# Kernel optimization log

Measured on AMD Instinct MI355X. Metric: run time of the kernel, lower is better.

The kernel has to match this reference:

```python
import jax, jax.numpy as jnp
import numpy as np

PAD_Y = 16
PAD_X = 16


def setup_inputs() -> dict:
    key = jax.random.key(0)
    k1, k2, k3, k4 = jax.random.split(key, 4)
    B, NLAM, H, W = 4, 96, 256, 256
    KS = 15
    cube = jax.random.normal(k1, (B, NLAM, H, W), dtype=jnp.float32)
    # per-(ksequence, wavelength) dispersion shifts in pixels (a few px)
    dx = 3.0 * jax.random.normal(k2, (4, NLAM), dtype=jnp.float32)
    dy = 3.0 * jax.random.normal(k3, (4, NLAM), dtype=jnp.float32)
    psf = jax.random.uniform(k4, (KS, KS), dtype=jnp.float32)
    psf = psf / psf.sum()  # normalised PSF as in the original
    return {"cube": cube, "dx": dx, "dy": dy, "psf_kernel": psf}


def _forward(cube, dx, dy, psf_kernel):
    B, n_lam, H, W = cube.shape
    H_out, W_out = H + 2 * PAD_Y, W + 2 * PAD_X
    padded = jnp.pad(cube, ((0, 0), (0, 0), (PAD_Y, PAD_Y), (PAD_X, PAD_X)))
    yy, xx = jnp.meshgrid(jnp.arange(H_out, dtype=cube.dtype),
                          jnp.arange(W_out, dtype=cube.dtype), indexing="ij")

    def shift_one(img_b, d_x, d_y):
        # img_b: (B, H_out, W_out); output[y,x] = input[y-dy, x-dx], bilinear,
        # zeros outside (matches grid_sample padding_mode='zeros', align_corners=True)
        coords = jnp.stack([yy - d_y, xx - d_x])  # (2, H_out, W_out)
        return jax.vmap(lambda im: jax.scipy.ndimage.map_coordinates(
            im, coords, order=1, mode="constant", cval=0.0))(img_b)

    def per_k(dxk, dyk):
        # vmap over wavelengths -> (n_lam, B, H_out, W_out); accumulate over lambda
        shifted = jax.vmap(shift_one, in_axes=(1, 0, 0))(padded, dxk, dyk)
        return shifted.sum(0)  # (B, H_out, W_out)

    acc = jax.vmap(per_k)(dx, dy)            # (4, B, H_out, W_out)
    acc = jnp.transpose(acc, (1, 0, 2, 3))   # (B, 4, H_out, W_out)

    # PSF conv (same kernel every channel); conv is linear so conv(sum) == sum(conv)
    ks = psf_kernel.shape[-1]
    p = ks // 2
    x = acc.reshape(B * 4, 1, H_out, W_out)
    kern = psf_kernel.reshape(1, 1, ks, ks)
    out = jax.lax.conv_general_dilated(
        x, kern, window_strides=(1, 1), padding=[(p, p), (p, p)],
        dimension_numbers=("NCHW", "OIHW", "NCHW"))
    return out.reshape(B, 4, H_out, W_out)


def reference(cube, dx, dy, psf_kernel):
    return _forward(cube, dx, dy, psf_kernel)
```

## Files before the change

### kernel.cpp

```cpp
#include <hip/hip_runtime.h>

#define BB 4
#define NLAM 96
#define HH 256
#define WW 256
#define HO 288
#define WO 288
#define NK 4
#define KS 15
#define PADK 7

#define ACC_N ((size_t)BB * NK * HO * WO)

#define SP 105
#define TILE_N (65 * SP)
#define SDUMMY TILE_N
#define NQ 7

typedef float f4 __attribute__((ext_vector_type(4), aligned(4)));
typedef float f4a __attribute__((ext_vector_type(4)));

__global__ __launch_bounds__(384) void params_k(const float* __restrict__ dx,
                                                const float* __restrict__ dy,
                                                float4* __restrict__ pw,
                                                int2* __restrict__ po,
                                                int4* __restrict__ gmm) {
    __shared__ int sox[384], soy[384];
    const int i = threadIdx.x;
    const float sx = -dx[i] - 16.0f;
    const float sy = -dy[i] - 16.0f;
    const float fx = floorf(sx), fy = floorf(sy);
    const int ox = (int)fx, oy = (int)fy;
    po[i] = make_int2(ox, oy);
    pw[i] = make_float4(1.0f - (sx - fx), sx - fx, 1.0f - (sy - fy), sy - fy);
    sox[i] = ox; soy[i] = oy;
    __syncthreads();
    if (i < 64) {
        int mnx = sox[i], mxx = mnx, mny = soy[i], mxy = mny;
        for (int j = i + 64; j < 384; j += 64) {
            mnx = min(mnx, sox[j]); mxx = max(mxx, sox[j]);
            mny = min(mny, soy[j]); mxy = max(mxy, soy[j]);
        }
        for (int m = 32; m; m >>= 1) {
            mnx = min(mnx, __shfl_xor(mnx, m, 64));
            mxx = max(mxx, __shfl_xor(mxx, m, 64));
            mny = min(mny, __shfl_xor(mny, m, 64));
            mxy = max(mxy, __shfl_xor(mxy, m, 64));
        }
        if (i == 0) *gmm = make_int4(mnx, mxx, mny, mxy);
    }
}

__global__ __launch_bounds__(256, 4) void shift_accum(
        const float* __restrict__ cube,
        const float4* __restrict__ pw,
        const int2* __restrict__ po,
        const int4* __restrict__ gmm,
        float* __restrict__ part,
        int S, int chunk) {
    __shared__ float tile[TILE_N + 8];
    const int zc  = blockIdx.z;
    const int b   = zc / S;
    const int c   = zc - b * S;
    const int tx0 = blockIdx.x * 64;
    const int ty0 = blockIdx.y * 32;
    const int tx  = threadIdx.x, ty = threadIdx.y;
    const int x   = tx0 + tx * 4;
    const int y   = ty0 + ty * 2;
    const int tid = ty * 16 + tx;
    const float* __restrict__ cb = cube + (size_t)b * NLAM * HH * WW;

    const int4 mm = *gmm;
    const int spanX = mm.y - mm.x;
    const int spanY = mm.w - mm.z;
    const bool lds_ok = (spanX <= 32) && (spanY <= 31);

    f4a a[NK][2];
#pragma unroll
    for (int k = 0; k < NK; ++k) { a[k][0] = (f4a)0.f; a[k][1] = (f4a)0.f; }

    const int l0 = min(NLAM, c * chunk);
    const int l1 = min(NLAM, l0 + chunk);

    if (lds_ok) {
        const int row0 = ty0 + mm.z;
        const int col0 = (tx0 + mm.x) & ~3;
        const int R    = spanY + 34;
        const int tb0  = (ty * 2 - mm.z) * SP + (tx * 4 + (tx0 - col0));

        int  goffB[NQ];
        int  waddr[NQ];
        float mf[NQ];
        int  pf = 0;
#pragma unroll
        for (int s = 0; s < NQ; ++s) {
            const int q  = tid + s * 256;
            const bool inR = q < R * 26;
            const int r  = q / 26;
            const int qi = q - r * 26;
            const int gy = row0 + r;
            const int gc = col0 + qi * 4;
            const bool rowOK = (unsigned)gy < (unsigned)HH;
            const bool fullQ = rowOK && gc >= 0 && gc <= WW - 4;
            const bool partQ = inR && rowOK && !fullQ && (gc + 3 >= 0) && (gc < WW);
            const int gyc = min(max(gy, 0), HH - 1);
            const int gcc = min(max(gc, 0), WW - 4);
            goffB[s] = (gyc * WW + gcc) * 4;
            mf[s]    = (inR && fullQ) ? 1.0f : 0.0f;
            waddr[s] = (inR && !partQ) ? (r * SP + qi * 4) : SDUMMY;
            if (partQ) pf |= 1 << s;
        }

        for (int i = tid; i < TILE_N + 8; i += 256) tile[i] = 0.0f;
        __syncthreads();

        for (int lam = l0; lam < l1; ++lam) {
            const char* __restrict__ ib = (const char*)(cb + lam * (HH * WW));
#pragma unroll
            for (int s = 0; s < NQ; ++s) {
                f4a v = *(const f4a*)(ib + goffB[s]);
                const float m = mf[s];
                const int wa = waddr[s];
                tile[wa]     = v.x * m;
                tile[wa + 1] = v.y * m;
                tile[wa + 2] = v.z * m;
                tile[wa + 3] = v.w * m;
            }
            if (pf) {
#pragma unroll
                for (int s = 0; s < NQ; ++s) {
                    if (pf & (1 << s)) {
                        const int q  = tid + s * 256;
                        const int r  = q / 26;
                        const int qi = q - r * 26;
                        const int gy = row0 + r;
                        const int gc = col0 + qi * 4;
                        const float* rp = (const float*)ib + gy * WW;
                        const int la = r * SP + qi * 4;
#pragma unroll
                        for (int e = 0; e < 4; ++e)
                            if ((unsigned)(gc + e) < (unsigned)WW)
                                tile[la + e] = rp[gc + e];
                    }
                }
            }
            __syncthreads();
#pragma unroll
            for (int k = 0; k < NK; ++k) {
                const int i_ = k * NLAM + lam;
                const int2 o = po[i_]; const float4 w = pw[i_];
                const float* t = tile + tb0 + o.y * SP + o.x;
                float t0[5], t1[5], t2[5];
#pragma unroll
                for (int cc = 0; cc < 5; ++cc) {
                    t0[cc] = t[cc];
                    t1[cc] = t[SP + cc];
                    t2[cc] = t[2 * SP + cc];
                }
                f4a r0 = {t0[0], t0[1], t0[2], t0[3]};
                f4a r1 = {t1[0], t1[1], t1[2], t1[3]};
                f4a r2 = {t2[0], t2[1], t2[2], t2[3]};
                f4a vb0 = w.z * r0 + w.w * r1;
                f4a vb1 = w.z * r1 + w.w * r2;
                const float e0 = w.z * t0[4] + w.w * t1[4];
                const float e1 = w.z * t1[4] + w.w * t2[4];
                f4a s0 = {vb0.y, vb0.z, vb0.w, e0};
                f4a s1 = {vb1.y, vb1.z, vb1.w, e1};
                a[k][0] += w.x * vb0 + w.y * s0;
                a[k][1] += w.x * vb1 + w.y * s1;
            }
            __syncthreads();
        }
    } else {
        for (int lam = l0; lam < l1; ++lam) {
            const float* __restrict__ img = cb + lam * (HH * WW);
#pragma unroll
            for (int k = 0; k < NK; ++k) {
                const int i_ = k * NLAM + lam;
                const int2 o = po[i_]; const float4 w = pw[i_];
#pragma unroll
                for (int j = 0; j < 2; ++j) {
                    const int iy = y + j + o.y;
                    const int ix = x + o.x;
                    const int cy0 = min(max(iy, 0), HH - 1);
                    const int cy1 = min(max(iy + 1, 0), HH - 1);
                    const float my0 = ((unsigned)iy       < (unsigned)HH) ? w.z : 0.0f;
                    const float my1 = ((unsigned)(iy + 1) < (unsigned)HH) ? w.w : 0.0f;
                    const float* r0p = img + cy0 * WW;
                    const float* r1p = img + cy1 * WW;
                    float rb[5];
#pragma unroll
                    for (int cc = 0; cc < 5; ++cc) {
                        const int cx = min(max(ix + cc, 0), WW - 1);
                        const float m = ((unsigned)(ix + cc) < (unsigned)WW) ? 1.0f : 0.0f;
                        rb[cc] = m * (my0 * r0p[cx] + my1 * r1p[cx]);
                    }
                    f4a d;
                    d.x = w.x * rb[0] + w.y * rb[1];
                    d.y = w.x * rb[1] + w.y * rb[2];
                    d.z = w.x * rb[2] + w.y * rb[3];
                    d.w = w.x * rb[3] + w.y * rb[4];
                    a[k][j] += d;
                }
            }
        }
    }

    if (x < WO) {
        const size_t hw = (size_t)HO * WO;
        float* pa = part + (size_t)c * ACC_N + ((size_t)(b * NK) * HO + y) * WO + x;
#pragma unroll
        for (int k = 0; k < NK; ++k) {
            *(f4a*)(pa + (size_t)k * hw)      = a[k][0];
            *(f4a*)(pa + (size_t)k * hw + WO) = a[k][1];
        }
    }
}

#define CPX 112
#define CROWS 30
#define CTILE_N (CROWS * CPX)
#define CDUMMY CTILE_N
#define NQC 5

template <int S>
__global__ __launch_bounds__(192) void conv_psf(const float* __restrict__ part,
                                                const float* __restrict__ psf,
                                                float* __restrict__ out) {
    __shared__ float tilec[CTILE_N + 8];
    __shared__ float spsf[KS][16];
    const int bk  = blockIdx.z;
    const int gx0 = blockIdx.x * 96 - PADK;
    const int gy0 = blockIdx.y * 16 - PADK;
    const float* __restrict__ ap = part + (size_t)bk * HO * WO;

    const int tid = threadIdx.y * 24 + threadIdx.x;
    for (int i = tid; i < KS * 16; i += 192) {
        const int r = i >> 4, cc2 = i & 15;
        spsf[r][cc2] = (cc2 < KS) ? psf[r * KS + cc2] : 0.0f;
    }

    int goffB[NQC], laddr[NQC];
    f4a cmask[NQC];
#pragma unroll
    for (int s = 0; s < NQC; ++s) {
        const int q  = tid + s * 192;
        const bool inR = q < CROWS * 28;
        const int r  = q / 28;
        const int qi = q - r * 28;
        const int gy = gy0 + r;
        const int gx = gx0 + qi * 4;
        const bool rowOK = (unsigned)gy < (unsigned)HO;
        const int gyc = min(max(gy, 0), HO - 1);
        goffB[s] = (gyc * WO + gx) * 4;
        laddr[s] = inR ? (r * CPX + qi * 4) : CDUMMY;
        f4a m;
#pragma unroll
        for (int e = 0; e < 4; ++e)
            m[e] = (inR && rowOK && (unsigned)(gx + e) < (unsigned)WO) ? 1.0f : 0.0f;
        cmask[s] = m;
    }

#pragma unroll
    for (int s = 0; s < NQC; ++s) {
        const char* base = (const char*)ap + goffB[s];
        f4a acc = (f4a)0.f;
#pragma unroll
        for (int cc = 0; cc < S; ++cc) {
            f4 v = *(const f4*)(base + (size_t)cc * (ACC_N * 4));
            acc += (f4a)v;
        }
        acc *= cmask[s];
        const int la = laddr[s];
        tilec[la] = acc.x; tilec[la + 1] = acc.y;
        tilec[la + 2] = acc.z; tilec[la + 3] = acc.w;
    }
    __syncthreads();

    const int x0 = threadIdx.x * 4;
    const int y0 = threadIdx.y * 2;
    f4a o0 = (f4a)0.f, o1 = (f4a)0.f;
    f4a prev0, prev1, prev2, prev3;

#pragma unroll
    for (int rr = 0; rr < 16; ++rr) {
        const float* rp = &tilec[(y0 + rr) * CPX + x0];
        float row[18];
#pragma unroll
        for (int q = 0; q < 4; ++q) {
            f4a v = *(const f4a*)(rp + 4 * q);
            row[4 * q]     = v.x; row[4 * q + 1] = v.y;
            row[4 * q + 2] = v.z; row[4 * q + 3] = v.w;
        }
        row[16] = rp[16]; row[17] = rp[17];

        f4a c0, c1, c2, c3;
        if (rr < 15) {
            c0 = *(const f4a*)&spsf[rr][0];
            c1 = *(const f4a*)&spsf[rr][4];
            c2 = *(const f4a*)&spsf[rr][8];
            c3 = *(const f4a*)&spsf[rr][12];
        }
        if (rr < 15) {
#pragma unroll
            for (int kx = 0; kx < KS; ++kx) {
                const float wv = (kx < 4) ? c0[kx] : (kx < 8) ? c1[kx - 4]
                               : (kx < 12) ? c2[kx - 8] : c3[kx - 12];
                f4a rv = {row[kx], row[kx + 1], row[kx + 2], row[kx + 3]};
                o0 += wv * rv;
            }
        }
        if (rr >= 1) {
#pragma unroll
            for (int kx = 0; kx < KS; ++kx) {
                const float wv = (kx < 4) ? prev0[kx] : (kx < 8) ? prev1[kx - 4]
                               : (kx < 12) ? prev2[kx - 8] : prev3[kx - 12];
                f4a rv = {row[kx], row[kx + 1], row[kx + 2], row[kx + 3]};
                o1 += wv * rv;
            }
        }
        prev0 = c0; prev1 = c1; prev2 = c2; prev3 = c3;
    }

    const int xo = blockIdx.x * 96 + x0;
    const int yo = blockIdx.y * 16 + y0;
    float* op = out + ((size_t)bk * HO + yo) * WO + xo;
    *(f4a*)op        = o0;
    *(f4a*)(op + WO) = o1;
}

extern "C" void kernel_launch(void* const* d_in, const int* in_sizes, int n_in,
                              void* d_out, int out_size, void* d_ws, size_t ws_size,
                              hipStream_t stream) {
    const float* cube = (const float*)d_in[0];
    const float* dx   = (const float*)d_in[1];
    const float* dy   = (const float*)d_in[2];
    const float* psf  = (const float*)d_in[3];
    float* out = (float*)d_out;

    const size_t ACCB   = ACC_N * sizeof(float);
    const size_t tables = 384 * sizeof(float4) + 384 * sizeof(int2) + sizeof(int4);

    int S = 1;
    for (int cand : {12, 8, 6, 4, 3, 2}) {
        if (ws_size >= 64 + (size_t)cand * ACCB + tables + 4096) { S = cand; break; }
    }
    const int chunk = (NLAM + S - 1) / S;

    float* part = (float*)((char*)d_ws + 64);
    char*  tb   = (char*)part + (size_t)S * ACCB;
    float4* pw  = (float4*)tb;
    int2*   po  = (int2*)(tb + 384 * sizeof(float4));
    int4*   gmm = (int4*)(tb + 384 * sizeof(float4) + 384 * sizeof(int2));

    params_k<<<1, 384, 0, stream>>>(dx, dy, pw, po, gmm);

    dim3 b1(16, 16);
    dim3 g1((WO + 63) / 64, HO / 32, BB * S);
    shift_accum<<<g1, b1, 0, stream>>>(cube, pw, po, gmm, part, S, chunk);

    dim3 b2(24, 8);
    dim3 g2(WO / 96, HO / 16, BB * NK);
    switch (S) {
        case 12: conv_psf<12><<<g2, b2, 0, stream>>>(part, psf, out); break;
        case 8:  conv_psf<8><<<g2, b2, 0, stream>>>(part, psf, out); break;
        case 6:  conv_psf<6><<<g2, b2, 0, stream>>>(part, psf, out); break;
        case 4:  conv_psf<4><<<g2, b2, 0, stream>>>(part, psf, out); break;
        case 3:  conv_psf<3><<<g2, b2, 0, stream>>>(part, psf, out); break;
        case 2:  conv_psf<2><<<g2, b2, 0, stream>>>(part, psf, out); break;
        default: conv_psf<1><<<g2, b2, 0, stream>>>(part, psf, out); break;
    }
}
```

Measured before the change: 226.8 us.

## Load cube tiles directly into LDS via global_load_lds and vectorize tile reads

The shift-accumulate kernel now streams cube tiles straight from global memory into LDS with the buffer-to-LDS load builtin, instead of staging them through registers. Out-of-range quads read from a zeroed scratch buffer, so the per-block zero fill and the dummy-address writes are gone. Tile reads become aligned 8-wide LDS loads with a wave-uniform switch on the sub-word offset. The PSF conv tile is realigned so rows load as full float4 vectors. In exchange, the code depends on the builtin's LDS layout and on the partial-quad path waiting explicitly on vmcnt, which adds ordering risk.

```diff
diff --git a/kernel.cpp b/kernel.cpp
--- a/kernel.cpp
+++ b/kernel.cpp
@@ -12,21 +12,22 @@
 
 #define ACC_N ((size_t)BB * NK * HO * WO)
 
-#define SP 105
-#define TILE_N (65 * SP)
-#define SDUMMY TILE_N
+#define SP 104
 #define NQ 7
-
-typedef float f4 __attribute__((ext_vector_type(4), aligned(4)));
+#define TILE_Q (NQ * 256)
+
 typedef float f4a __attribute__((ext_vector_type(4)));
+typedef float f8v __attribute__((ext_vector_type(8), aligned(16)));
 
 __global__ __launch_bounds__(384) void params_k(const float* __restrict__ dx,
                                                 const float* __restrict__ dy,
                                                 float4* __restrict__ pw,
                                                 int2* __restrict__ po,
-                                                int4* __restrict__ gmm) {
+                                                int4* __restrict__ gmm,
+                                                float* __restrict__ zp) {
     __shared__ int sox[384], soy[384];
     const int i = threadIdx.x;
+    if (i < 32) zp[i] = 0.0f;
     const float sx = -dx[i] - 16.0f;
     const float sy = -dy[i] - 16.0f;
     const float fx = floorf(sx), fy = floorf(sy);
@@ -51,14 +52,30 @@
     }
 }
 
+#define GATH(P)                                                          \
+    {                                                                    \
+        f4a r0 = {R0[P], R0[(P)+1], R0[(P)+2], R0[(P)+3]};               \
+        f4a r1 = {R1[P], R1[(P)+1], R1[(P)+2], R1[(P)+3]};               \
+        f4a r2 = {R2[P], R2[(P)+1], R2[(P)+2], R2[(P)+3]};               \
+        f4a vb0 = w.z * r0 + w.w * r1;                                   \
+        f4a vb1 = w.z * r1 + w.w * r2;                                   \
+        const float e0 = w.z * R0[(P)+4] + w.w * R1[(P)+4];              \
+        const float e1 = w.z * R1[(P)+4] + w.w * R2[(P)+4];              \
+        f4a s0 = {vb0.y, vb0.z, vb0.w, e0};                              \
+        f4a s1 = {vb1.y, vb1.z, vb1.w, e1};                              \
+        a[k][0] += w.x * vb0 + w.y * s0;                                 \
+        a[k][1] += w.x * vb1 + w.y * s1;                                 \
+    }
+
 __global__ __launch_bounds__(256, 4) void shift_accum(
         const float* __restrict__ cube,
         const float4* __restrict__ pw,
         const int2* __restrict__ po,
         const int4* __restrict__ gmm,
+        const float* __restrict__ zp,
         float* __restrict__ part,
         int S, int chunk) {
-    __shared__ float tile[TILE_N + 8];
+    __shared__ __align__(16) float tile[TILE_Q * 4 + 8];
     const int zc  = blockIdx.z;
     const int b   = zc / S;
     const int c   = zc - b * S;
@@ -86,47 +103,52 @@
         const int row0 = ty0 + mm.z;
         const int col0 = (tx0 + mm.x) & ~3;
         const int R    = spanY + 34;
-        const int tb0  = (ty * 2 - mm.z) * SP + (tx * 4 + (tx0 - col0));
-
-        int  goffB[NQ];
-        int  waddr[NQ];
-        float mf[NQ];
-        int  pf = 0;
+        const int Rq   = R * 26;
+        const int dx0  = tx0 - col0;
+        const int tb0  = (ty * 2 - mm.z) * SP + tx * 4 + dx0;
+        const int ldsq0 = tid & 192;
+        const char* zpc = (const char*)zp;
+
+        int goffB[NQ];
+        int fm = 0;
+        int pf = 0;
 #pragma unroll
         for (int s = 0; s < NQ; ++s) {
             const int q  = tid + s * 256;
-            const bool inR = q < R * 26;
+            const bool inR = q < Rq;
             const int r  = q / 26;
             const int qi = q - r * 26;
             const int gy = row0 + r;
             const int gc = col0 + qi * 4;
             const bool rowOK = (unsigned)gy < (unsigned)HH;
-            const bool fullQ = rowOK && gc >= 0 && gc <= WW - 4;
+            const bool fullQ = inR && rowOK && gc >= 0 && gc <= WW - 4;
             const bool partQ = inR && rowOK && !fullQ && (gc + 3 >= 0) && (gc < WW);
-            const int gyc = min(max(gy, 0), HH - 1);
-            const int gcc = min(max(gc, 0), WW - 4);
-            goffB[s] = (gyc * WW + gcc) * 4;
-            mf[s]    = (inR && fullQ) ? 1.0f : 0.0f;
-            waddr[s] = (inR && !partQ) ? (r * SP + qi * 4) : SDUMMY;
+            goffB[s] = (gy * WW + gc) * 4;
+            if (fullQ) fm |= 1 << s;
             if (partQ) pf |= 1 << s;
         }
-
-        for (int i = tid; i < TILE_N + 8; i += 256) tile[i] = 0.0f;
-        __syncthreads();
 
         for (int lam = l0; lam < l1; ++lam) {
             const char* __restrict__ ib = (const char*)(cb + lam * (HH * WW));
 #pragma unroll
             for (int s = 0; s < NQ; ++s) {
-                f4a v = *(const f4a*)(ib + goffB[s]);
-                const float m = mf[s];
-                const int wa = waddr[s];
-                tile[wa]     = v.x * m;
-                tile[wa + 1] = v.y * m;
-                tile[wa + 2] = v.z * m;
-                tile[wa + 3] = v.w * m;
+                if (s * 256 < Rq) {
+                    const char* src = ((fm >> s) & 1) ? (ib + goffB[s]) : zpc;
+                    __builtin_amdgcn_global_load_lds(
+                        (const __attribute__((address_space(1))) unsigned int*)src,
+                        (__attribute__((address_space(3))) unsigned int*)
+                            (tile + (s * 256 + ldsq0) * 4),
+                        16, 0, 0);
+                }
+            }
+            int2 ok[NK]; float4 wk[NK];
+#pragma unroll
+            for (int k = 0; k < NK; ++k) {
+                ok[k] = po[k * NLAM + lam];
+                wk[k] = pw[k * NLAM + lam];
             }
             if (pf) {
+                asm volatile("s_waitcnt vmcnt(0)" ::: "memory");
 #pragma unroll
                 for (int s = 0; s < NQ; ++s) {
                     if (pf & (1 << s)) {
@@ -139,35 +161,27 @@
                         const int la = r * SP + qi * 4;
 #pragma unroll
                         for (int e = 0; e < 4; ++e)
-                            if ((unsigned)(gc + e) < (unsigned)WW)
-                                tile[la + e] = rp[gc + e];
+                            tile[la + e] = ((unsigned)(gc + e) < (unsigned)WW)
+                                               ? rp[gc + e] : 0.0f;
                     }
                 }
             }
             __syncthreads();
 #pragma unroll
             for (int k = 0; k < NK; ++k) {
-                const int i_ = k * NLAM + lam;
-                const int2 o = po[i_]; const float4 w = pw[i_];
-                const float* t = tile + tb0 + o.y * SP + o.x;
-                float t0[5], t1[5], t2[5];
-#pragma unroll
-                for (int cc = 0; cc < 5; ++cc) {
-                    t0[cc] = t[cc];
-                    t1[cc] = t[SP + cc];
-                    t2[cc] = t[2 * SP + cc];
+                const int2 o = ok[k]; const float4 w = wk[k];
+                const int bidx = tb0 + o.y * SP + o.x;
+                const int p = __builtin_amdgcn_readfirstlane(bidx & 3);
+                const float* ta = tile + (bidx & ~3);
+                const f8v R0 = *(const f8v*)ta;
+                const f8v R1 = *(const f8v*)(ta + SP);
+                const f8v R2 = *(const f8v*)(ta + 2 * SP);
+                switch (p) {
+                    case 0:  GATH(0); break;
+                    case 1:  GATH(1); break;
+                    case 2:  GATH(2); break;
+                    default: GATH(3); break;
                 }
-                f4a r0 = {t0[0], t0[1], t0[2], t0[3]};
-                f4a r1 = {t1[0], t1[1], t1[2], t1[3]};
-                f4a r2 = {t2[0], t2[1], t2[2], t2[3]};
-                f4a vb0 = w.z * r0 + w.w * r1;
-                f4a vb1 = w.z * r1 + w.w * r2;
-                const float e0 = w.z * t0[4] + w.w * t1[4];
-                const float e1 = w.z * t1[4] + w.w * t2[4];
-                f4a s0 = {vb0.y, vb0.z, vb0.w, e0};
-                f4a s1 = {vb1.y, vb1.z, vb1.w, e1};
-                a[k][0] += w.x * vb0 + w.y * s0;
-                a[k][1] += w.x * vb1 + w.y * s1;
             }
             __syncthreads();
         }
@@ -220,17 +234,16 @@
 #define CPX 112
 #define CROWS 30
 #define CTILE_N (CROWS * CPX)
-#define CDUMMY CTILE_N
 #define NQC 5
 
 template <int S>
 __global__ __launch_bounds__(192) void conv_psf(const float* __restrict__ part,
                                                 const float* __restrict__ psf,
                                                 float* __restrict__ out) {
-    __shared__ float tilec[CTILE_N + 8];
-    __shared__ float spsf[KS][16];
+    __shared__ __align__(16) float tilec[CTILE_N + 16];
+    __shared__ __align__(16) float spsf[KS][16];
     const int bk  = blockIdx.z;
-    const int gx0 = blockIdx.x * 96 - PADK;
+    const int gx0 = blockIdx.x * 96 - 8;
     const int gy0 = blockIdx.y * 16 - PADK;
     const float* __restrict__ ap = part + (size_t)bk * HO * WO;
 
@@ -253,7 +266,7 @@
         const bool rowOK = (unsigned)gy < (unsigned)HO;
         const int gyc = min(max(gy, 0), HO - 1);
         goffB[s] = (gyc * WO + gx) * 4;
-        laddr[s] = inR ? (r * CPX + qi * 4) : CDUMMY;
+        laddr[s] = inR ? (r * CPX + qi * 4) : CTILE_N;
         f4a m;
 #pragma unroll
         for (int e = 0; e < 4; ++e)
@@ -266,14 +279,10 @@
         const char* base = (const char*)ap + goffB[s];
         f4a acc = (f4a)0.f;
 #pragma unroll
-        for (int cc = 0; cc < S; ++cc) {
-            f4 v = *(const f4*)(base + (size_t)cc * (ACC_N * 4));
-            acc += (f4a)v;
-        }
+        for (int cc = 0; cc < S; ++cc)
+            acc += *(const f4a*)(base + (size_t)cc * (ACC_N * 4));
         acc *= cmask[s];
-        const int la = laddr[s];
-        tilec[la] = acc.x; tilec[la + 1] = acc.y;
-        tilec[la + 2] = acc.z; tilec[la + 3] = acc.w;
+        *(f4a*)(tilec + laddr[s]) = acc;
     }
     __syncthreads();
 
@@ -285,14 +294,13 @@
 #pragma unroll
     for (int rr = 0; rr < 16; ++rr) {
         const float* rp = &tilec[(y0 + rr) * CPX + x0];
-        float row[18];
-#pragma unroll
-        for (int q = 0; q < 4; ++q) {
+        float row[20];
+#pragma unroll
+        for (int q = 0; q < 5; ++q) {
             f4a v = *(const f4a*)(rp + 4 * q);
             row[4 * q]     = v.x; row[4 * q + 1] = v.y;
             row[4 * q + 2] = v.z; row[4 * q + 3] = v.w;
         }
-        row[16] = rp[16]; row[17] = rp[17];
 
         f4a c0, c1, c2, c3;
         if (rr < 15) {
@@ -306,7 +314,7 @@
             for (int kx = 0; kx < KS; ++kx) {
                 const float wv = (kx < 4) ? c0[kx] : (kx < 8) ? c1[kx - 4]
                                : (kx < 12) ? c2[kx - 8] : c3[kx - 12];
-                f4a rv = {row[kx], row[kx + 1], row[kx + 2], row[kx + 3]};
+                f4a rv = {row[kx + 1], row[kx + 2], row[kx + 3], row[kx + 4]};
                 o0 += wv * rv;
             }
         }
@@ -315,7 +323,7 @@
             for (int kx = 0; kx < KS; ++kx) {
                 const float wv = (kx < 4) ? prev0[kx] : (kx < 8) ? prev1[kx - 4]
                                : (kx < 12) ? prev2[kx - 8] : prev3[kx - 12];
-                f4a rv = {row[kx], row[kx + 1], row[kx + 2], row[kx + 3]};
+                f4a rv = {row[kx + 1], row[kx + 2], row[kx + 3], row[kx + 4]};
                 o1 += wv * rv;
             }
         }
@@ -343,21 +351,22 @@
 
     int S = 1;
     for (int cand : {12, 8, 6, 4, 3, 2}) {
-        if (ws_size >= 64 + (size_t)cand * ACCB + tables + 4096) { S = cand; break; }
+        if (ws_size >= 128 + (size_t)cand * ACCB + tables + 4096) { S = cand; break; }
     }
     const int chunk = (NLAM + S - 1) / S;
 
-    float* part = (float*)((char*)d_ws + 64);
+    float* zp   = (float*)d_ws;
+    float* part = (float*)((char*)d_ws + 128);
     char*  tb   = (char*)part + (size_t)S * ACCB;
     float4* pw  = (float4*)tb;
     int2*   po  = (int2*)(tb + 384 * sizeof(float4));
     int4*   gmm = (int4*)(tb + 384 * sizeof(float4) + 384 * sizeof(int2));
 
-    params_k<<<1, 384, 0, stream>>>(dx, dy, pw, po, gmm);
+    params_k<<<1, 384, 0, stream>>>(dx, dy, pw, po, gmm, zp);
 
     dim3 b1(16, 16);
     dim3 g1((WO + 63) / 64, HO / 32, BB * S);
-    shift_accum<<<g1, b1, 0, stream>>>(cube, pw, po, gmm, part, S, chunk);
+    shift_accum<<<g1, b1, 0, stream>>>(cube, pw, po, gmm, zp, part, S, chunk);
 
     dim3 b2(24, 8);
     dim3 g2(WO / 96, HO / 16, BB * NK);
```

Measured after the change: 618.4 us. +172.6%, slower.
